# Optimization experiments

Hardware: AMD Instinct MI355X
Metric: run time of the kernel (lower is better)

## Reference

```python
import jax, jax.numpy as jnp
import numpy as np

B, P, C = 256, 256, 512
EPS = 1e-6

def setup_inputs() -> dict:
    key = jax.random.key(0)
    ks = jax.random.split(key, 9)
    s_p = 1.0 / np.sqrt(P)
    s_c = 1.0 / np.sqrt(C)
    return {
        "x": jax.random.normal(ks[0], (B, P, C), dtype=jnp.float32),
        "ln_g": jnp.ones((C,), jnp.float32),
        "ln_b": jnp.zeros((C,), jnp.float32),
        # token-mixing MLP (P -> P -> P)
        "w1a": jax.random.normal(ks[1], (P, P), jnp.float32) * s_p,
        "b1a": jnp.zeros((P,), jnp.float32),
        "w1b": jax.random.normal(ks[2], (P, P), jnp.float32) * s_p,
        "b1b": jnp.zeros((P,), jnp.float32),
        # channel-mixing MLP (C -> C -> C)
        "w2a": jax.random.normal(ks[3], (C, C), jnp.float32) * s_c,
        "b2a": jnp.zeros((C,), jnp.float32),
        "w2b": jax.random.normal(ks[4], (C, C), jnp.float32) * s_c,
        "b2b": jnp.zeros((C,), jnp.float32),
    }

def _layernorm(v, g, b):
    mu = jnp.mean(v, axis=-1, keepdims=True)
    var = jnp.mean(jnp.square(v - mu), axis=-1, keepdims=True)
    return (v - mu) * jax.lax.rsqrt(var + EPS) * g + b

def reference(x, ln_g, ln_b, w1a, b1a, w1b, b1b, w2a, b2a, w2b, b2b):
    # token mixing: normalize, transpose to [B, C, P], MLP over P, transpose back
    h = _layernorm(x, ln_g, ln_b)                       # [B, P, C]
    ht = jnp.swapaxes(h, 1, 2)                          # [B, C, P]
    t = jax.nn.gelu(ht @ w1a + b1a, approximate=False) @ w1b + b1b
    x = jnp.swapaxes(t, 1, 2) + x                       # residual with original input
    # channel mixing: note residual adds to the NORMALIZED x (as in source)
    h = _layernorm(x, ln_g, ln_b)                       # [B, P, C]
    t2 = jax.nn.gelu(h @ w2a + b2a, approximate=False) @ w2b + b2b
    return h + t2
```

## Files before the change

### kernel.cpp

```cpp
#include <hip/hip_runtime.h>
#include <hip/hip_bf16.h>
#include <math.h>

typedef __bf16 bf16x8 __attribute__((ext_vector_type(8)));
typedef float f32x4 __attribute__((ext_vector_type(4)));
typedef unsigned short u16x8 __attribute__((ext_vector_type(8)));

#define DEV __device__ __forceinline__

DEV unsigned short f2bf(float f){ __hip_bfloat16 h=__float2bfloat16(f); unsigned short u; __builtin_memcpy(&u,&h,2); return u; }
DEV float bf2f(unsigned short u){ __hip_bfloat16 h; __builtin_memcpy(&h,&u,2); return __bfloat162float(h); }

DEV float gelu_f(float v){
  float u = v*(0.7978845608f + 0.0356774081f*v*v);
  float e = __expf(2.0f*u);
  float t = 1.0f - 2.0f*__builtin_amdgcn_rcpf(e + 1.0f);
  return 0.5f*v*(1.0f + t);
}

DEV void gl2lds16(const void* g, void* l){
  __builtin_amdgcn_global_load_lds((const __attribute__((address_space(1))) void*)g,
                                   (__attribute__((address_space(3))) void*)l, 16, 0, 0);
}

__global__ __launch_bounds__(256) void k_wtt(const float* __restrict__ w1a,
                                             const float* __restrict__ w1b,
                                             const float* __restrict__ w2a,
                                             const float* __restrict__ w2b,
                                             unsigned short* __restrict__ o1a,
                                             unsigned short* __restrict__ o1b,
                                             unsigned short* __restrict__ o2a,
                                             unsigned short* __restrict__ o2b){
  __shared__ float tl[64][65];
  int bid = blockIdx.x;
  const float* W; unsigned short* O; int NN, tile_id;
  if (bid < 16)      { W = w1a; O = o1a; NN = 256; tile_id = bid; }
  else if (bid < 32) { W = w1b; O = o1b; NN = 256; tile_id = bid - 16; }
  else if (bid < 96) { W = w2a; O = o2a; NN = 512; tile_id = bid - 32; }
  else               { W = w2b; O = o2b; NN = 512; tile_id = bid - 96; }
  int tpr = NN >> 6;
  int tr = tile_id / tpr, tc = tile_id % tpr;
  int tid = threadIdx.x;
  int r = tid >> 2, cseg = (tid & 3) << 4;
  #pragma unroll
  for (int j = 0; j < 4; ++j){
    float4 v = *(const float4*)(W + (size_t)(tr*64 + r)*NN + tc*64 + cseg + j*4);
    tl[r][cseg + j*4 + 0] = v.x;
    tl[r][cseg + j*4 + 1] = v.y;
    tl[r][cseg + j*4 + 2] = v.z;
    tl[r][cseg + j*4 + 3] = v.w;
  }
  __syncthreads();
  int rn = tid >> 2, kseg = (tid & 3) << 4;
  #pragma unroll
  for (int h = 0; h < 2; ++h){
    u16x8 o;
    #pragma unroll
    for (int j = 0; j < 8; ++j) o[j] = f2bf(tl[kseg + h*8 + j][rn]);
    *(u16x8*)(O + (size_t)(tc*64 + rn)*NN + tr*64 + kseg + h*8) = o;
  }
}

__global__ __launch_bounds__(512) void k_ln1x(const float* __restrict__ x,
                                              const float* __restrict__ g,
                                              const float* __restrict__ be,
                                              unsigned short* __restrict__ ht,
                                              unsigned short* __restrict__ xb){
  __shared__ unsigned short tile[32][512];
  int blk = blockIdx.x;
  int b = blk >> 3, p0 = (blk & 7) << 5;
  int tid = threadIdx.x, w = tid >> 6, l = tid & 63;
  float4 gv0 = *(const float4*)(g  + l*8);
  float4 gv1 = *(const float4*)(g  + l*8 + 4);
  float4 bv0 = *(const float4*)(be + l*8);
  float4 bv1 = *(const float4*)(be + l*8 + 4);
  const float* xbase = x + (((size_t)b << 8) + p0) * 512;
  #pragma unroll
  for (int i = 0; i < 4; ++i){
    int pl = (i << 3) + w;
    const float* row = xbase + (size_t)pl*512 + l*8;
    float4 v0 = *(const float4*)row;
    float4 v1 = *(const float4*)(row + 4);
    u16x8 rc;
    rc[0]=f2bf(v0.x); rc[1]=f2bf(v0.y); rc[2]=f2bf(v0.z); rc[3]=f2bf(v0.w);
    rc[4]=f2bf(v1.x); rc[5]=f2bf(v1.y); rc[6]=f2bf(v1.z); rc[7]=f2bf(v1.w);
    *(u16x8*)(xb + (((size_t)b << 8) + p0 + pl)*512 + l*8) = rc;
    float s  = v0.x+v0.y+v0.z+v0.w + v1.x+v1.y+v1.z+v1.w;
    float s2 = v0.x*v0.x+v0.y*v0.y+v0.z*v0.z+v0.w*v0.w
             + v1.x*v1.x+v1.y*v1.y+v1.z*v1.z+v1.w*v1.w;
    #pragma unroll
    for (int off = 32; off; off >>= 1){ s += __shfl_xor(s, off); s2 += __shfl_xor(s2, off); }
    float mu = s * (1.0f/512.0f);
    float rs = rsqrtf(s2*(1.0f/512.0f) - mu*mu + 1e-6f);
    u16x8 o;
    o[0]=f2bf((v0.x-mu)*rs*gv0.x+bv0.x);
    o[1]=f2bf((v0.y-mu)*rs*gv0.y+bv0.y);
    o[2]=f2bf((v0.z-mu)*rs*gv0.z+bv0.z);
    o[3]=f2bf((v0.w-mu)*rs*gv0.w+bv0.w);
    o[4]=f2bf((v1.x-mu)*rs*gv1.x+bv1.x);
    o[5]=f2bf((v1.y-mu)*rs*gv1.y+bv1.y);
    o[6]=f2bf((v1.z-mu)*rs*gv1.z+bv1.z);
    o[7]=f2bf((v1.w-mu)*rs*gv1.w+bv1.w);
    *(u16x8*)(&tile[pl][(l ^ ((pl >> 3) << 1)) << 3]) = o;
  }
  __syncthreads();
  unsigned short* hb = ht + ((size_t)b << 17);
  #pragma unroll
  for (int it = 0; it < 4; ++it){
    int c = (it << 7) + (tid >> 2);
    int q = tid & 3, pch = q << 3;
    int cs = c ^ (q << 4);
    u16x8 o;
    #pragma unroll
    for (int j = 0; j < 8; ++j) o[j] = tile[pch + j][cs];
    *(u16x8*)(hb + (size_t)c*256 + p0 + pch) = o;
  }
}

__global__ __launch_bounds__(256) void k_tl2s(const unsigned short* __restrict__ t,
                                              const unsigned short* __restrict__ xb,
                                              const float* __restrict__ g,
                                              const float* __restrict__ be,
                                              unsigned short* __restrict__ h2){
  int tid = threadIdx.x, w = tid >> 6, l = tid & 63;
  float4 gv0 = *(const float4*)(g  + l*8);
  float4 gv1 = *(const float4*)(g  + l*8 + 4);
  float4 bv0 = *(const float4*)(be + l*8);
  float4 bv1 = *(const float4*)(be + l*8 + 4);
  int r = blockIdx.x*4 + w;
  size_t off = (size_t)r*512 + l*8;
  u16x8 tv = *(const u16x8*)(t + off);
  u16x8 xv = *(const u16x8*)(xb + off);
  float v[8];
  #pragma unroll
  for (int j = 0; j < 8; ++j) v[j] = bf2f(tv[j]) + bf2f(xv[j]);
  float s = 0.f, s2 = 0.f;
  #pragma unroll
  for (int j = 0; j < 8; ++j){ s += v[j]; s2 += v[j]*v[j]; }
  #pragma unroll
  for (int o2 = 32; o2; o2 >>= 1){ s += __shfl_xor(s, o2); s2 += __shfl_xor(s2, o2); }
  float mu = s * (1.0f/512.0f);
  float rs = rsqrtf(s2*(1.0f/512.0f) - mu*mu + 1e-6f);
  u16x8 o;
  o[0]=f2bf((v[0]-mu)*rs*gv0.x+bv0.x);
  o[1]=f2bf((v[1]-mu)*rs*gv0.y+bv0.y);
  o[2]=f2bf((v[2]-mu)*rs*gv0.z+bv0.z);
  o[3]=f2bf((v[3]-mu)*rs*gv0.w+bv0.w);
  o[4]=f2bf((v[4]-mu)*rs*gv1.x+bv1.x);
  o[5]=f2bf((v[5]-mu)*rs*gv1.y+bv1.y);
  o[6]=f2bf((v[6]-mu)*rs*gv1.z+bv1.z);
  o[7]=f2bf((v[7]-mu)*rs*gv1.w+bv1.w);
  *(u16x8*)(h2 + off) = o;
}

template<int N, int KT, int MODE>
__global__ __launch_bounds__(256, 2) void k_gemm(
    const unsigned short* __restrict__ A,
    const unsigned short* __restrict__ BT,
    const float* __restrict__ bias,
    unsigned short* __restrict__ outb,
    float* __restrict__ outf,
    const unsigned short* __restrict__ res)
{
  constexpr int K = KT*64;
  constexpr int nTn = N/128;
  constexpr int EPITCH = 176;
  constexpr int EREG   = 64*EPITCH;
  __shared__ char lds[4*EREG];
  char* lsA = lds;
  char* lsB = lds + 16384;

  int nwg = gridDim.x, bid = blockIdx.x;
  int wgid = ((nwg & 7) == 0) ? ((bid & 7)*(nwg >> 3) + (bid >> 3)) : bid;
  int tm = wgid / nTn, tn = wgid % nTn;
  size_t m0 = (size_t)tm * 128;
  int n0 = tn * 128;

  const int tid = threadIdx.x;
  const int w = tid >> 6, l = tid & 63;
  const int wm = w >> 1, wn = w & 1;
  const int la = l & 15, lg = l >> 4;

  f32x4 acc[4][4];
  #pragma unroll
  for (int i = 0; i < 4; ++i)
    #pragma unroll
    for (int j = 0; j < 4; ++j) acc[i][j] = (f32x4){0.f,0.f,0.f,0.f};

  for (int kt = 0; kt < KT; ++kt){
    int kb = kt << 6;
    #pragma unroll
    for (int i = 0; i < 4; ++i){
      int q = (i << 8) + tid;
      int row = q >> 3, sc = q & 7;
      int cc = sc ^ (row & 7);
      gl2lds16(A  + (m0 + row)*K + kb + (cc << 3), lsA + q*16);
      gl2lds16(BT + (size_t)(n0 + row)*K + kb + (cc << 3), lsB + q*16);
    }
    __syncthreads();
    #pragma unroll
    for (int ks = 0; ks < 2; ++ks){
      int c = (ks << 2) + lg;
      bf16x8 af[4], bfr[4];
      #pragma unroll
      for (int mi = 0; mi < 4; ++mi){
        int rr = (wm << 6) + (mi << 4) + la;
        af[mi] = *(const bf16x8*)(lsA + ((rr << 3) + (c ^ (rr & 7)))*16);
      }
      #pragma unroll
      for (int ni = 0; ni < 4; ++ni){
        int rn = (wn << 6) + (ni << 4) + la;
        bfr[ni] = *(const bf16x8*)(lsB + ((rn << 3) + (c ^ (rn & 7)))*16);
      }
      #pragma unroll
      for (int mi = 0; mi < 4; ++mi)
        #pragma unroll
        for (int ni = 0; ni < 4; ++ni)
          acc[mi][ni] = __builtin_amdgcn_mfma_f32_16x16x32_bf16(af[mi], bfr[ni], acc[mi][ni], 0, 0, 0);
    }
    __syncthreads();
  }

  char* ep = lds + w*EREG;
  #pragma unroll
  for (int ni = 0; ni < 4; ++ni){
    int colw = (ni << 4) + la;
    float bv = bias[n0 + (wn << 6) + colw];
    #pragma unroll
    for (int mi = 0; mi < 4; ++mi){
      #pragma unroll
      for (int rg = 0; rg < 4; ++rg){
        float v = acc[mi][ni][rg] + bv;
        if (MODE == 0) v = gelu_f(v);
        int r = (mi << 4) + (lg << 2) + rg;
        *(unsigned short*)(ep + r*EPITCH + colw*2) = f2bf(v);
      }
    }
  }
  __syncthreads();

  #pragma unroll
  for (int i = 0; i < 8; ++i){
    int q = (i << 8) + tid;
    int r = q >> 4, ck = q & 15;
    int wreg = ((r >> 6) << 1) | (ck >> 3);
    u16x8 val = *(const u16x8*)(lds + wreg*EREG + (r & 63)*EPITCH + (ck & 7)*16);
    size_t go = (m0 + r)*N + n0 + (ck << 3);
    if (MODE != 2){
      *(u16x8*)(outb + go) = val;
    } else {
      u16x8 rv = *(const u16x8*)(res + go);
      float4 o0, o1;
      o0.x = bf2f(val[0]) + bf2f(rv[0]);
      o0.y = bf2f(val[1]) + bf2f(rv[1]);
      o0.z = bf2f(val[2]) + bf2f(rv[2]);
      o0.w = bf2f(val[3]) + bf2f(rv[3]);
      o1.x = bf2f(val[4]) + bf2f(rv[4]);
      o1.y = bf2f(val[5]) + bf2f(rv[5]);
      o1.z = bf2f(val[6]) + bf2f(rv[6]);
      o1.w = bf2f(val[7]) + bf2f(rv[7]);
      *(float4*)(outf + go)     = o0;
      *(float4*)(outf + go + 4) = o1;
    }
  }
}

__global__ __launch_bounds__(256, 2) void k_gemmT(
    const unsigned short* __restrict__ A,
    const unsigned short* __restrict__ BT,
    const float* __restrict__ bias,
    unsigned short* __restrict__ outb)
{
  constexpr int K = 256, KT = 4;
  constexpr int EPITCH = 176;
  constexpr int EREG   = 64*EPITCH;
  __shared__ char lds[4*EREG];
  char* lsA = lds;
  char* lsB = lds + 16384;

  int nwg = gridDim.x, bid = blockIdx.x;
  int wgid = (bid & 7)*(nwg >> 3) + (bid >> 3);
  int tm = wgid & 1, tn = wgid >> 1;
  size_t m0 = (size_t)tm * 128;
  int n0 = tn * 128;
  int bb = n0 >> 9, c0 = n0 & 511;

  const int tid = threadIdx.x;
  const int w = tid >> 6, l = tid & 63;
  const int wm = w >> 1, wn = w & 1;
  const int la = l & 15, lg = l >> 4;

  f32x4 acc[4][4];
  #pragma unroll
  for (int i = 0; i < 4; ++i)
    #pragma unroll
    for (int j = 0; j < 4; ++j) acc[i][j] = (f32x4){0.f,0.f,0.f,0.f};

  for (int kt = 0; kt < KT; ++kt){
    int kb = kt << 6;
    #pragma unroll
    for (int i = 0; i < 4; ++i){
      int q = (i << 8) + tid;
      int row = q >> 3, sc = q & 7;
      int cc = sc ^ (row & 7);
      gl2lds16(A  + (m0 + row)*K + kb + (cc << 3), lsA + q*16);
      gl2lds16(BT + (size_t)(n0 + row)*K + kb + (cc << 3), lsB + q*16);
    }
    __syncthreads();
    #pragma unroll
    for (int ks = 0; ks < 2; ++ks){
      int c = (ks << 2) + lg;
      bf16x8 af[4], bfr[4];
      #pragma unroll
      for (int mi = 0; mi < 4; ++mi){
        int rr = (wm << 6) + (mi << 4) + la;
        af[mi] = *(const bf16x8*)(lsA + ((rr << 3) + (c ^ (rr & 7)))*16);
      }
      #pragma unroll
      for (int ni = 0; ni < 4; ++ni){
        int rn = (wn << 6) + (ni << 4) + la;
        bfr[ni] = *(const bf16x8*)(lsB + ((rn << 3) + (c ^ (rn & 7)))*16);
      }
      #pragma unroll
      for (int mi = 0; mi < 4; ++mi)
        #pragma unroll
        for (int ni = 0; ni < 4; ++ni)
          acc[mi][ni] = __builtin_amdgcn_mfma_f32_16x16x32_bf16(af[mi], bfr[ni], acc[mi][ni], 0, 0, 0);
    }
    __syncthreads();
  }

  char* ep = lds + w*EREG;
  #pragma unroll
  for (int mi = 0; mi < 4; ++mi){
    int rb = (mi << 4) + (lg << 2);
    float4 bq = *(const float4*)(bias + m0 + (wm << 6) + rb);
    #pragma unroll
    for (int ni = 0; ni < 4; ++ni){
      int colw = (ni << 4) + la;
      #pragma unroll
      for (int rg = 0; rg < 4; ++rg){
        float v = acc[mi][ni][rg] + ((const float*)&bq)[rg];
        *(unsigned short*)(ep + (rb + rg)*EPITCH + colw*2) = f2bf(v);
      }
    }
  }
  __syncthreads();

  #pragma unroll
  for (int i = 0; i < 8; ++i){
    int q = (i << 8) + tid;
    int r = q >> 4, ck = q & 15;
    int wreg = ((r >> 6) << 1) | (ck >> 3);
    u16x8 val = *(const u16x8*)(lds + wreg*EREG + (r & 63)*EPITCH + (ck & 7)*16);
    size_t go = ((size_t)bb << 17) + (m0 + r)*512 + c0 + (ck << 3);
    *(u16x8*)(outb + go) = val;
  }
}

extern "C" void kernel_launch(void* const* d_in, const int* in_sizes, int n_in,
                              void* d_out, int out_size, void* d_ws, size_t ws_size,
                              hipStream_t stream) {
  const float* x   = (const float*)d_in[0];
  const float* lng = (const float*)d_in[1];
  const float* lnb = (const float*)d_in[2];
  const float* w1a = (const float*)d_in[3];
  const float* b1a = (const float*)d_in[4];
  const float* w1b = (const float*)d_in[5];
  const float* b1b = (const float*)d_in[6];
  const float* w2a = (const float*)d_in[7];
  const float* b2a = (const float*)d_in[8];
  const float* w2b = (const float*)d_in[9];
  const float* b2b = (const float*)d_in[10];
  float* out = (float*)d_out;
  char* ws = (char*)d_ws;
  unsigned short* bufA = (unsigned short*)ws;
  unsigned short* bufB = (unsigned short*)(ws + (size_t)(64u << 20));
  unsigned short* wt1a = (unsigned short*)(ws + (size_t)(128u << 20));
  unsigned short* wt1b = wt1a + 256*256;
  unsigned short* wt2a = wt1b + 256*256;
  unsigned short* wt2b = wt2a + 512*512;
  unsigned short* xb   = (unsigned short*)d_out;

  k_wtt<<<160, 256, 0, stream>>>(w1a, w1b, w2a, w2b, wt1a, wt1b, wt2a, wt2b);

  k_ln1x<<<2048, 512, 0, stream>>>(x, lng, lnb, bufA, xb);
  k_gemm<256, 4, 0><<<2048, 256, 0, stream>>>(bufA, wt1a, b1a, bufB, nullptr, nullptr);
  k_gemmT<<<2048, 256, 0, stream>>>(wt1b, bufB, b1b, bufA);

  k_tl2s<<<16384, 256, 0, stream>>>(bufA, xb, lng, lnb, bufB);

  k_gemm<512, 8, 0><<<2048, 256, 0, stream>>>(bufB, wt2a, b2a, bufA, nullptr, nullptr);
  k_gemm<512, 8, 2><<<2048, 256, 0, stream>>>(bufA, wt2b, b2b, nullptr, out, bufB);
}
```

Measured before the change: 272.1 us.

## Fuse token-mixing MLP's two GEMMs into one kernel with LDS-resident intermediate

Replaces the separate token-mixing GEMM (with GELU) and the transposed second GEMM with a single kernel. Each block computes a 64-row slab of the hidden activation, keeps the GELU output in LDS, then runs the second GEMM against it and writes the result back in [B,P,C] layout. This removes a full round trip of the intermediate through global memory and one kernel launch. In exchange each block reloads both full 256x256 weight matrices, and the larger LDS footprint (about 77KB) may limit occupancy.

```diff
diff --git a/kernel.cpp b/kernel.cpp
--- a/kernel.cpp
+++ b/kernel.cpp
@@ -138,7 +138,7 @@
   #pragma unroll
   for (int j = 0; j < 8; ++j){ s += v[j]; s2 += v[j]*v[j]; }
   #pragma unroll
-  for (int o2 = 32; o2; o2 >>= 1){ s += __shfl_xor(s, o2); s2 += __shfl_xor(s2, o2); }
+  for (int o2i = 32; o2i; o2i >>= 1){ s += __shfl_xor(s, o2i); s2 += __shfl_xor(s2, o2i); }
   float mu = s * (1.0f/512.0f);
   float rs = rsqrtf(s2*(1.0f/512.0f) - mu*mu + 1e-6f);
   u16x8 o;
@@ -151,6 +151,146 @@
   o[6]=f2bf((v[6]-mu)*rs*gv1.z+bv1.z);
   o[7]=f2bf((v[7]-mu)*rs*gv1.w+bv1.w);
   *(u16x8*)(h2 + off) = o;
+}
+
+__global__ __launch_bounds__(256, 2) void k_tok(
+    const unsigned short* __restrict__ ht,
+    const unsigned short* __restrict__ w1aT,
+    const unsigned short* __restrict__ w1bT,
+    const float* __restrict__ b1a,
+    const float* __restrict__ b1b,
+    unsigned short* __restrict__ t)
+{
+  constexpr int EPITCH = 144;
+  __shared__ char lsA[8192];
+  __shared__ char lsW[EPITCH*256];
+  __shared__ char Ul[32768];
+
+  int nwg = gridDim.x, bid = blockIdx.x;
+  int wgid = (bid & 7)*(nwg >> 3) + (bid >> 3);
+  size_t bc0 = (size_t)wgid * 64;
+  int b = (int)(bc0 >> 9), c0 = (int)(bc0 & 511);
+
+  const int tid = threadIdx.x;
+  const int w = tid >> 6, l = tid & 63;
+  const int la = l & 15, lg = l >> 4;
+
+  f32x4 acc[4][4];
+  #pragma unroll
+  for (int i = 0; i < 4; ++i)
+    #pragma unroll
+    for (int j = 0; j < 4; ++j) acc[i][j] = (f32x4){0.f,0.f,0.f,0.f};
+
+  for (int kt = 0; kt < 4; ++kt){
+    int kb = kt << 6;
+    #pragma unroll
+    for (int i = 0; i < 2; ++i){
+      int q = (i << 8) + tid;
+      int row = q >> 3, sc = q & 7, cc = sc ^ (row & 7);
+      gl2lds16(ht + (bc0 + row)*256 + kb + (cc << 3), lsA + q*16);
+    }
+    #pragma unroll
+    for (int i = 0; i < 8; ++i){
+      int q = (i << 8) + tid;
+      int row = q >> 3, sc = q & 7, cc = sc ^ (row & 7);
+      gl2lds16(w1aT + (size_t)row*256 + kb + (cc << 3), lsW + q*16);
+    }
+    __syncthreads();
+    #pragma unroll
+    for (int ks = 0; ks < 2; ++ks){
+      int c = (ks << 2) + lg;
+      bf16x8 af[4], bfr[4];
+      #pragma unroll
+      for (int mi = 0; mi < 4; ++mi){
+        int rr = (mi << 4) + la;
+        af[mi] = *(const bf16x8*)(lsA + ((rr << 3) + (c ^ (rr & 7)))*16);
+      }
+      #pragma unroll
+      for (int ni = 0; ni < 4; ++ni){
+        int rn = (w << 6) + (ni << 4) + la;
+        bfr[ni] = *(const bf16x8*)(lsW + ((rn << 3) + (c ^ (rn & 7)))*16);
+      }
+      #pragma unroll
+      for (int mi = 0; mi < 4; ++mi)
+        #pragma unroll
+        for (int ni = 0; ni < 4; ++ni)
+          acc[mi][ni] = __builtin_amdgcn_mfma_f32_16x16x32_bf16(af[mi], bfr[ni], acc[mi][ni], 0, 0, 0);
+    }
+    __syncthreads();
+  }
+  #pragma unroll
+  for (int ni = 0; ni < 4; ++ni){
+    int p1 = (w << 6) + (ni << 4) + la;
+    float bv = b1a[p1];
+    int ckW = p1 >> 3, cw = p1 & 7;
+    #pragma unroll
+    for (int mi = 0; mi < 4; ++mi){
+      #pragma unroll
+      for (int rg = 0; rg < 4; ++rg){
+        int bcr = (mi << 4) + (lg << 2) + rg;
+        float v = gelu_f(acc[mi][ni][rg] + bv);
+        *(unsigned short*)(Ul + (size_t)bcr*512 + (((ckW ^ (bcr & 7)) << 4) + (cw << 1))) = f2bf(v);
+        acc[mi][ni][rg] = 0.0f;
+      }
+    }
+  }
+  __syncthreads();
+
+  for (int kt2 = 0; kt2 < 4; ++kt2){
+    int kb = kt2 << 6;
+    #pragma unroll
+    for (int i = 0; i < 8; ++i){
+      int q = (i << 8) + tid;
+      int row = q >> 3, sc = q & 7, cc = sc ^ (row & 7);
+      gl2lds16(w1bT + (size_t)row*256 + kb + (cc << 3), lsW + q*16);
+    }
+    __syncthreads();
+    #pragma unroll
+    for (int ks = 0; ks < 2; ++ks){
+      int cch = (ks << 2) + lg;
+      int cki = (kt2 << 3) + cch;
+      bf16x8 af[4], bfr[4];
+      #pragma unroll
+      for (int mi = 0; mi < 4; ++mi){
+        int rp = (w << 6) + (mi << 4) + la;
+        af[mi] = *(const bf16x8*)(lsW + ((rp << 3) + (cch ^ (rp & 7)))*16);
+      }
+      #pragma unroll
+      for (int ni = 0; ni < 4; ++ni){
+        int rbc = (ni << 4) + la;
+        bfr[ni] = *(const bf16x8*)(Ul + (((size_t)rbc << 5) + (cki ^ (rbc & 7)))*16);
+      }
+      #pragma unroll
+      for (int mi = 0; mi < 4; ++mi)
+        #pragma unroll
+        for (int ni = 0; ni < 4; ++ni)
+          acc[mi][ni] = __builtin_amdgcn_mfma_f32_16x16x32_bf16(af[mi], bfr[ni], acc[mi][ni], 0, 0, 0);
+    }
+    __syncthreads();
+  }
+
+  #pragma unroll
+  for (int mi = 0; mi < 4; ++mi){
+    int rb = (w << 6) + (mi << 4) + (lg << 2);
+    float4 bq = *(const float4*)(b1b + rb);
+    #pragma unroll
+    for (int ni = 0; ni < 4; ++ni){
+      int col = (ni << 4) + la;
+      #pragma unroll
+      for (int rg = 0; rg < 4; ++rg){
+        float v = acc[mi][ni][rg] + ((const float*)&bq)[rg];
+        *(unsigned short*)(lsW + (rb + rg)*EPITCH + col*2) = f2bf(v);
+      }
+    }
+  }
+  __syncthreads();
+  #pragma unroll
+  for (int i = 0; i < 8; ++i){
+    int q = (i << 8) + tid;
+    int r = q >> 3, ck = q & 7;
+    u16x8 val = *(const u16x8*)(lsW + r*EPITCH + ck*16);
+    *(u16x8*)(t + ((size_t)b << 17) + (size_t)r*512 + c0 + (ck << 3)) = val;
+  }
 }
 
 template<int N, int KT, int MODE>
@@ -262,99 +402,6 @@
       *(float4*)(outf + go)     = o0;
       *(float4*)(outf + go + 4) = o1;
     }
-  }
-}
-
-__global__ __launch_bounds__(256, 2) void k_gemmT(
-    const unsigned short* __restrict__ A,
-    const unsigned short* __restrict__ BT,
-    const float* __restrict__ bias,
-    unsigned short* __restrict__ outb)
-{
-  constexpr int K = 256, KT = 4;
-  constexpr int EPITCH = 176;
-  constexpr int EREG   = 64*EPITCH;
-  __shared__ char lds[4*EREG];
-  char* lsA = lds;
-  char* lsB = lds + 16384;
-
-  int nwg = gridDim.x, bid = blockIdx.x;
-  int wgid = (bid & 7)*(nwg >> 3) + (bid >> 3);
-  int tm = wgid & 1, tn = wgid >> 1;
-  size_t m0 = (size_t)tm * 128;
-  int n0 = tn * 128;
-  int bb = n0 >> 9, c0 = n0 & 511;
-
-  const int tid = threadIdx.x;
-  const int w = tid >> 6, l = tid & 63;
-  const int wm = w >> 1, wn = w & 1;
-  const int la = l & 15, lg = l >> 4;
-
-  f32x4 acc[4][4];
-  #pragma unroll
-  for (int i = 0; i < 4; ++i)
-    #pragma unroll
-    for (int j = 0; j < 4; ++j) acc[i][j] = (f32x4){0.f,0.f,0.f,0.f};
-
-  for (int kt = 0; kt < KT; ++kt){
-    int kb = kt << 6;
-    #pragma unroll
-    for (int i = 0; i < 4; ++i){
-      int q = (i << 8) + tid;
-      int row = q >> 3, sc = q & 7;
-      int cc = sc ^ (row & 7);
-      gl2lds16(A  + (m0 + row)*K + kb + (cc << 3), lsA + q*16);
-      gl2lds16(BT + (size_t)(n0 + row)*K + kb + (cc << 3), lsB + q*16);
-    }
-    __syncthreads();
-    #pragma unroll
-    for (int ks = 0; ks < 2; ++ks){
-      int c = (ks << 2) + lg;
-      bf16x8 af[4], bfr[4];
-      #pragma unroll
-      for (int mi = 0; mi < 4; ++mi){
-        int rr = (wm << 6) + (mi << 4) + la;
-        af[mi] = *(const bf16x8*)(lsA + ((rr << 3) + (c ^ (rr & 7)))*16);
-      }
-      #pragma unroll
-      for (int ni = 0; ni < 4; ++ni){
-        int rn = (wn << 6) + (ni << 4) + la;
-        bfr[ni] = *(const bf16x8*)(lsB + ((rn << 3) + (c ^ (rn & 7)))*16);
-      }
-      #pragma unroll
-      for (int mi = 0; mi < 4; ++mi)
-        #pragma unroll
-        for (int ni = 0; ni < 4; ++ni)
-          acc[mi][ni] = __builtin_amdgcn_mfma_f32_16x16x32_bf16(af[mi], bfr[ni], acc[mi][ni], 0, 0, 0);
-    }
-    __syncthreads();
-  }
-
-  char* ep = lds + w*EREG;
-  #pragma unroll
-  for (int mi = 0; mi < 4; ++mi){
-    int rb = (mi << 4) + (lg << 2);
-    float4 bq = *(const float4*)(bias + m0 + (wm << 6) + rb);
-    #pragma unroll
-    for (int ni = 0; ni < 4; ++ni){
-      int colw = (ni << 4) + la;
-      #pragma unroll
-      for (int rg = 0; rg < 4; ++rg){
-        float v = acc[mi][ni][rg] + ((const float*)&bq)[rg];
-        *(unsigned short*)(ep + (rb + rg)*EPITCH + colw*2) = f2bf(v);
-      }
-    }
-  }
-  __syncthreads();
-
-  #pragma unroll
-  for (int i = 0; i < 8; ++i){
-    int q = (i << 8) + tid;
-    int r = q >> 4, ck = q & 15;
-    int wreg = ((r >> 6) << 1) | (ck >> 3);
-    u16x8 val = *(const u16x8*)(lds + wreg*EREG + (r & 63)*EPITCH + (ck & 7)*16);
-    size_t go = ((size_t)bb << 17) + (m0 + r)*512 + c0 + (ck << 3);
-    *(u16x8*)(outb + go) = val;
   }
 }
 
@@ -385,11 +432,10 @@
   k_wtt<<<160, 256, 0, stream>>>(w1a, w1b, w2a, w2b, wt1a, wt1b, wt2a, wt2b);
 
   k_ln1x<<<2048, 512, 0, stream>>>(x, lng, lnb, bufA, xb);
-  k_gemm<256, 4, 0><<<2048, 256, 0, stream>>>(bufA, wt1a, b1a, bufB, nullptr, nullptr);
-  k_gemmT<<<2048, 256, 0, stream>>>(wt1b, bufB, b1b, bufA);
-
-  k_tl2s<<<16384, 256, 0, stream>>>(bufA, xb, lng, lnb, bufB);
-
-  k_gemm<512, 8, 0><<<2048, 256, 0, stream>>>(bufB, wt2a, b2a, bufA, nullptr, nullptr);
-  k_gemm<512, 8, 2><<<2048, 256, 0, stream>>>(bufA, wt2b, b2b, nullptr, out, bufB);
-}
+  k_tok<<<2048, 256, 0, stream>>>(bufA, wt1a, wt1b, b1a, b1b, bufB);
+
+  k_tl2s<<<16384, 256, 0, stream>>>(bufB, xb, lng, lnb, bufA);
+
+  k_gemm<512, 8, 0><<<2048, 256, 0, stream>>>(bufA, wt2a, b2a, bufB, nullptr, nullptr);
+  k_gemm<512, 8, 2><<<2048, 256, 0, stream>>>(bufB, wt2b, b2b, nullptr, out, bufA);
+}
```

After: 269.7 us. No clear change (-0.9%).
